# Optimization experiments

Hardware: AMD Instinct MI355X
Metric: run time of the kernel (lower is better)

Reference implementation:

```python
import jax, jax.numpy as jnp
import numpy as np


def _maxpool2(t):
    # 2x2x2 max pool, stride 2. t: [B, C, D, H, W]
    B, C, D, H, W = t.shape
    return t.reshape(B, C, D // 2, 2, H // 2, 2, W // 2, 2).max(axis=(3, 5, 7))


def setup_inputs() -> dict:
    key = jax.random.key(0)
    ks = jax.random.split(key, 5)
    ch = 64
    B, D, H, W = 2, 32, 32, 32
    x = jax.random.normal(ks[0], (B, ch, D, H, W), dtype=jnp.float32)
    # 1x1x1 conv weights (out_ch, in_ch), Kaiming-ish scale
    w_theta = jax.random.normal(ks[1], (ch // 8, ch), dtype=jnp.float32) / np.sqrt(ch)
    w_phi = jax.random.normal(ks[2], (ch // 8, ch), dtype=jnp.float32) / np.sqrt(ch)
    w_g = jax.random.normal(ks[3], (ch // 2, ch), dtype=jnp.float32) / np.sqrt(ch)
    w_o = jax.random.normal(ks[4], (ch, ch // 2), dtype=jnp.float32) / np.sqrt(ch // 2)
    gamma = jnp.ones((), dtype=jnp.float32)  # original inits at 0; 1 gives nontrivial output
    return {"x": x, "w_theta": w_theta, "w_phi": w_phi, "w_g": w_g, "w_o": w_o, "gamma": gamma}


def reference(x, w_theta, w_phi, w_g, w_o, gamma):
    B, C, D, H, W = x.shape
    N = D * H * W
    M = N // 8
    xf = x.reshape(B, C, N)  # [B, C, N]
    # 1x1x1 convs = channel matmuls
    theta = jnp.einsum('oc,bcn->bon', w_theta, xf)                     # [B, C//8, N]
    phi = _maxpool2(jnp.einsum('oc,bcn->bon', w_phi, xf).reshape(B, C // 8, D, H, W)).reshape(B, C // 8, M)
    g = _maxpool2(jnp.einsum('oc,bcn->bon', w_g, xf).reshape(B, C // 2, D, H, W)).reshape(B, C // 2, M)
    # unscaled attention: softmax over keys (M)
    beta = jax.nn.softmax(jnp.einsum('bcn,bcm->bnm', theta, phi), axis=-1)  # [B, N, M]
    o = jnp.einsum('bcm,bnm->bcn', g, beta)                                 # [B, C//2, N]
    out = gamma * jnp.einsum('oc,bcn->bon', w_o, o).reshape(B, C, D, H, W) + x
    return out
```

## Files before the change

kernel.cpp:

```cpp
#include <hip/hip_runtime.h>
#include <cstdint>
#include <cstddef>

typedef __attribute__((ext_vector_type(4))) short short4v;
typedef __attribute__((ext_vector_type(4))) float float4v;

#define C_IN  64
#define NB    2
#define NPTS  32768
#define MPTS  4096
#define LOG2E 1.44269504088896340736f
#define KT    64
#define NTILE (MPTS / KT)
#define QT64  (NPTS / 64)

__device__ __forceinline__ unsigned short f2bf_rne(float f) {
  unsigned int u = __builtin_bit_cast(unsigned int, f);
  u += 0x7fffu + ((u >> 16) & 1u);
  return (unsigned short)(u >> 16);
}

__device__ __forceinline__ short4v pack_bf16_trunc(float a0, float a1, float a2, float a3) {
  unsigned int u0 = __builtin_amdgcn_perm(__builtin_bit_cast(unsigned int, a1),
                                          __builtin_bit_cast(unsigned int, a0), 0x07060302u);
  unsigned int u1 = __builtin_amdgcn_perm(__builtin_bit_cast(unsigned int, a3),
                                          __builtin_bit_cast(unsigned int, a2), 0x07060302u);
  union { unsigned int u[2]; short4v s; } r;
  r.u[0] = u0; r.u[1] = u1;
  return r.s;
}

__device__ __forceinline__ short4v pack_bf16_rne(float a0, float a1, float a2, float a3) {
  short4v s;
  s[0] = (short)f2bf_rne(a0); s[1] = (short)f2bf_rne(a1);
  s[2] = (short)f2bf_rne(a2); s[3] = (short)f2bf_rne(a3);
  return s;
}

__device__ __forceinline__ uint2 pack_bf16x4_u2(float4v a) {
  uint2 r;
  r.x = (unsigned int)f2bf_rne(a[0]) | ((unsigned int)f2bf_rne(a[1]) << 16);
  r.y = (unsigned int)f2bf_rne(a[2]) | ((unsigned int)f2bf_rne(a[3]) << 16);
  return r;
}

__device__ __forceinline__ void unpack_bf16x4_add(uint2 u, float4v* a) {
  (*a)[0] += __builtin_bit_cast(float, u.x << 16);
  (*a)[1] += __builtin_bit_cast(float, u.x & 0xffff0000u);
  (*a)[2] += __builtin_bit_cast(float, u.y << 16);
  (*a)[3] += __builtin_bit_cast(float, u.y & 0xffff0000u);
}

__device__ __forceinline__ void gl_lds16(const unsigned short* g, unsigned short* l) {
  __builtin_amdgcn_global_load_lds(
      (const __attribute__((address_space(1))) void*)g,
      (__attribute__((address_space(3))) void*)l, 16, 0, 0);
}


__device__ void pool_body(int idx, const float* __restrict__ x,
                          const float* __restrict__ w_phi,
                          const float* __restrict__ w_g,
                          unsigned short* __restrict__ phi_f,
                          unsigned short* __restrict__ g_f) {
  int cg = idx >> 13;
  int bm = idx & 8191;
  int b = bm >> 12, m = bm & 4095;
  int md = m >> 8, mh = (m >> 4) & 15, mw = m & 15;
  const float* xb = x + (size_t)b * C_IN * NPTS
                  + ((md * 2) * 1024 + (mh * 2) * 32 + (mw * 2));
  const float* wbase = (cg < 2) ? (w_phi + cg * 4 * C_IN)
                                : (w_g + (cg - 2) * 4 * C_IN);

  float acc[4][8];
#pragma unroll
  for (int o = 0; o < 4; ++o)
#pragma unroll
    for (int p = 0; p < 8; ++p) acc[o][p] = 0.f;

#pragma unroll 4
  for (int cc = 0; cc < C_IN; ++cc) {
    const float* xp = xb + (size_t)cc * NPTS;
    float2 p01 = *(const float2*)(xp + 0);
    float2 p23 = *(const float2*)(xp + 32);
    float2 p45 = *(const float2*)(xp + 1024);
    float2 p67 = *(const float2*)(xp + 1056);
#pragma unroll
    for (int o = 0; o < 4; ++o) {
      float wv = wbase[o * C_IN + cc];
      acc[o][0] = fmaf(wv, p01.x, acc[o][0]);
      acc[o][1] = fmaf(wv, p01.y, acc[o][1]);
      acc[o][2] = fmaf(wv, p23.x, acc[o][2]);
      acc[o][3] = fmaf(wv, p23.y, acc[o][3]);
      acc[o][4] = fmaf(wv, p45.x, acc[o][4]);
      acc[o][5] = fmaf(wv, p45.y, acc[o][5]);
      acc[o][6] = fmaf(wv, p67.x, acc[o][6]);
      acc[o][7] = fmaf(wv, p67.y, acc[o][7]);
    }
  }
  float mx[4];
#pragma unroll
  for (int o = 0; o < 4; ++o) {
    mx[o] = fmaxf(fmaxf(fmaxf(acc[o][0], acc[o][1]), fmaxf(acc[o][2], acc[o][3])),
                  fmaxf(fmaxf(acc[o][4], acc[o][5]), fmaxf(acc[o][6], acc[o][7])));
  }
  int kt16 = m >> 4, kr = m & 15;
  if (cg < 2) {
    size_t fb = ((size_t)b * 256 + kt16) * 256;
    unsigned int u0 = (unsigned int)f2bf_rne(mx[0] * LOG2E)
                    | ((unsigned int)f2bf_rne(mx[1] * LOG2E) << 16);
    unsigned int u1 = (unsigned int)f2bf_rne(mx[2] * LOG2E)
                    | ((unsigned int)f2bf_rne(mx[3] * LOG2E) << 16);
    *(uint2*)&phi_f[fb + (cg * 16 + kr) * 4] = make_uint2(u0, u1);
    *(uint2*)&phi_f[fb + ((cg + 2) * 16 + kr) * 4] = make_uint2(0u, 0u);
  } else {
    int gc0 = (cg - 2) * 4;
#pragma unroll
    for (int o = 0; o < 4; ++o) {
      int c = gc0 + o;
      int half = c >> 4, c15 = c & 15;
      size_t base = (((size_t)b * 256 + kt16) * 2 + half) * 256;
      g_f[base + ((kr >> 2) * 16 + c15) * 4 + (kr & 3)] = f2bf_rne(mx[o]);
    }
  }
}

__device__ void theta_body(int idx, const float* __restrict__ x,
                           const float* __restrict__ w_theta,
                           unsigned short* __restrict__ theta_pad) {
  int b = idx >> 15, n = idx & 32767;
  const float* xb = x + (size_t)b * C_IN * NPTS + n;
  float t[8];
#pragma unroll
  for (int o = 0; o < 8; ++o) t[o] = 0.f;
#pragma unroll 4
  for (int cc = 0; cc < C_IN; ++cc) {
    float xv = xb[(size_t)cc * NPTS];
#pragma unroll
    for (int o = 0; o < 8; ++o) t[o] = fmaf(w_theta[o * C_IN + cc], xv, t[o]);
  }
  unsigned int w0 = (unsigned int)f2bf_rne(t[0]) | ((unsigned int)f2bf_rne(t[1]) << 16);
  unsigned int w1 = (unsigned int)f2bf_rne(t[2]) | ((unsigned int)f2bf_rne(t[3]) << 16);
  unsigned int w2 = (unsigned int)f2bf_rne(t[4]) | ((unsigned int)f2bf_rne(t[5]) << 16);
  unsigned int w3 = (unsigned int)f2bf_rne(t[6]) | ((unsigned int)f2bf_rne(t[7]) << 16);
  uint4* dst = (uint4*)(theta_pad + ((size_t)idx << 4));
  dst[0] = make_uint4(w0, w1, w2, w3);
  dst[1] = make_uint4(0u, 0u, 0u, 0u);
}

__global__ __launch_bounds__(256) void prep_fused(
    const float* __restrict__ x, const float* __restrict__ w_theta,
    const float* __restrict__ w_phi, const float* __restrict__ w_g,
    unsigned short* __restrict__ theta_pad,
    unsigned short* __restrict__ phi_f,
    unsigned short* __restrict__ g_f) {
  int gb = blockIdx.x;
  if (gb < 320) {
    pool_body(gb * 256 + threadIdx.x, x, w_phi, w_g, phi_f, g_f);
  } else {
    theta_body((gb - 320) * 256 + threadIdx.x, x, w_theta, theta_pad);
  }
}

template <int KS>
__global__ __launch_bounds__(256, 4) void attn_split64(
    const unsigned short* __restrict__ theta_pad,
    const unsigned short* __restrict__ phi_f,
    const unsigned short* __restrict__ g_f,
    uint2* __restrict__ opart,
    float* __restrict__ lbuf) {
  __shared__ unsigned short s_phi[2][KT * 16];
  __shared__ unsigned short s_g[2][(KT / 16) * 512];

  int tid = threadIdx.x;
  int wid = tid >> 6, lane = tid & 63;
  int l4 = lane >> 4, col = lane & 15;
  int b = blockIdx.y / KS;
  int ks = blockIdx.y % KS;
  int qb = blockIdx.x * 256 + wid * 64;
  int qt64 = blockIdx.x * 4 + wid;
  int t0 = ks * (NTILE / KS);
  int t1 = t0 + NTILE / KS;

  const unsigned short* tb = theta_pad + ((size_t)(b * NPTS + qb) << 4) + l4 * 4;
  short4v bt0 = *(const short4v*)(tb + ((0 * 16 + col) << 4));
  short4v bt1 = *(const short4v*)(tb + ((1 * 16 + col) << 4));
  short4v bt2 = *(const short4v*)(tb + ((2 * 16 + col) << 4));
  short4v bt3 = *(const short4v*)(tb + ((3 * 16 + col) << 4));

  const unsigned short* phib = phi_f + (size_t)b * 65536;
  const unsigned short* gb   = g_f + (size_t)b * 131072;

  float4v acc[2][4];
#pragma unroll
  for (int h = 0; h < 2; ++h)
#pragma unroll
    for (int j = 0; j < 4; ++j) acc[h][j] = (float4v){0.f, 0.f, 0.f, 0.f};
  float lsum0 = 0.f, lsum1 = 0.f, lsum2 = 0.f, lsum3 = 0.f;

  gl_lds16(gb + (size_t)t0 * 2048 + wid * 512 + lane * 8, &s_g[0][wid * 512]);
  if (wid < 2)
    gl_lds16(phib + (size_t)t0 * 1024 + wid * 512 + lane * 8, &s_phi[0][wid * 512]);
  __syncthreads();

#pragma unroll 1
  for (int t = t0; t < t1; ++t) {
    int cur = t & 1;
    if (t + 1 < t1) {
      gl_lds16(gb + (size_t)(t + 1) * 2048 + wid * 512 + lane * 8,
               &s_g[cur ^ 1][wid * 512]);
      if (wid < 2)
        gl_lds16(phib + (size_t)(t + 1) * 1024 + wid * 512 + lane * 8,
                 &s_phi[cur ^ 1][wid * 512]);
    }

#pragma unroll
    for (int st = 0; st < 4; ++st) {
      short4v pf = *(const short4v*)&s_phi[cur][st * 256 + lane * 4];
      short4v g0 = *(const short4v*)&s_g[cur][st * 512 + lane * 4];
      short4v g1 = *(const short4v*)&s_g[cur][st * 512 + 256 + lane * 4];

      float4v zero4 = {0.f, 0.f, 0.f, 0.f};
      float4v s0 = __builtin_amdgcn_mfma_f32_16x16x16bf16_1k(pf, bt0, zero4, 0, 0, 0);
      float4v s1 = __builtin_amdgcn_mfma_f32_16x16x16bf16_1k(pf, bt1, zero4, 0, 0, 0);
      float4v s2 = __builtin_amdgcn_mfma_f32_16x16x16bf16_1k(pf, bt2, zero4, 0, 0, 0);
      float4v s3 = __builtin_amdgcn_mfma_f32_16x16x16bf16_1k(pf, bt3, zero4, 0, 0, 0);

      float p00 = __builtin_amdgcn_exp2f(s0[0]);
      float p01 = __builtin_amdgcn_exp2f(s0[1]);
      float p02 = __builtin_amdgcn_exp2f(s0[2]);
      float p03 = __builtin_amdgcn_exp2f(s0[3]);
      float p10 = __builtin_amdgcn_exp2f(s1[0]);
      float p11 = __builtin_amdgcn_exp2f(s1[1]);
      float p12 = __builtin_amdgcn_exp2f(s1[2]);
      float p13 = __builtin_amdgcn_exp2f(s1[3]);
      float p20 = __builtin_amdgcn_exp2f(s2[0]);
      float p21 = __builtin_amdgcn_exp2f(s2[1]);
      float p22 = __builtin_amdgcn_exp2f(s2[2]);
      float p23 = __builtin_amdgcn_exp2f(s2[3]);
      float p30 = __builtin_amdgcn_exp2f(s3[0]);
      float p31 = __builtin_amdgcn_exp2f(s3[1]);
      float p32 = __builtin_amdgcn_exp2f(s3[2]);
      float p33 = __builtin_amdgcn_exp2f(s3[3]);
      lsum0 += (p00 + p01) + (p02 + p03);
      lsum1 += (p10 + p11) + (p12 + p13);
      lsum2 += (p20 + p21) + (p22 + p23);
      lsum3 += (p30 + p31) + (p32 + p33);
      short4v pb0 = pack_bf16_trunc(p00, p01, p02, p03);
      short4v pb1 = pack_bf16_trunc(p10, p11, p12, p13);
      short4v pb2 = pack_bf16_trunc(p20, p21, p22, p23);
      short4v pb3 = pack_bf16_trunc(p30, p31, p32, p33);

      acc[0][0] = __builtin_amdgcn_mfma_f32_16x16x16bf16_1k(g0, pb0, acc[0][0], 0, 0, 0);
      acc[0][1] = __builtin_amdgcn_mfma_f32_16x16x16bf16_1k(g0, pb1, acc[0][1], 0, 0, 0);
      acc[0][2] = __builtin_amdgcn_mfma_f32_16x16x16bf16_1k(g0, pb2, acc[0][2], 0, 0, 0);
      acc[0][3] = __builtin_amdgcn_mfma_f32_16x16x16bf16_1k(g0, pb3, acc[0][3], 0, 0, 0);
      acc[1][0] = __builtin_amdgcn_mfma_f32_16x16x16bf16_1k(g1, pb0, acc[1][0], 0, 0, 0);
      acc[1][1] = __builtin_amdgcn_mfma_f32_16x16x16bf16_1k(g1, pb1, acc[1][1], 0, 0, 0);
      acc[1][2] = __builtin_amdgcn_mfma_f32_16x16x16bf16_1k(g1, pb2, acc[1][2], 0, 0, 0);
      acc[1][3] = __builtin_amdgcn_mfma_f32_16x16x16bf16_1k(g1, pb3, acc[1][3], 0, 0, 0);
    }
    __syncthreads();
  }

  lsum0 += __shfl_xor(lsum0, 16, 64);
  lsum0 += __shfl_xor(lsum0, 32, 64);
  lsum1 += __shfl_xor(lsum1, 16, 64);
  lsum1 += __shfl_xor(lsum1, 32, 64);
  lsum2 += __shfl_xor(lsum2, 16, 64);
  lsum2 += __shfl_xor(lsum2, 32, 64);
  lsum3 += __shfl_xor(lsum3, 16, 64);
  lsum3 += __shfl_xor(lsum3, 32, 64);

  size_t rowb = (size_t)(b * KS + ks) * QT64 + qt64;
  float myl = (l4 == 0) ? lsum0 : (l4 == 1) ? lsum1 : (l4 == 2) ? lsum2 : lsum3;
  lbuf[rowb * 64 + lane] = myl;

  size_t obase = rowb * 8 * 64 + lane;
#pragma unroll
  for (int h = 0; h < 2; ++h)
#pragma unroll
    for (int j = 0; j < 4; ++j)
      opart[obase + (size_t)(h * 4 + j) * 64] = pack_bf16x4_u2(acc[h][j]);
}

template <int KS>
__global__ __launch_bounds__(256) void attn_combine(
    const float* __restrict__ x, const float* __restrict__ w_o,
    const float* __restrict__ gamma_p,
    const uint2* __restrict__ opart,
    const float* __restrict__ lbuf,
    float* __restrict__ out) {
  int tid = threadIdx.x;
  int wid = tid >> 6, lane = tid & 63;
  int l4 = lane >> 4, col = lane & 15;
  int b = blockIdx.y;
  int qt32 = blockIdx.x * 4 + wid;
  int qb = qt32 * 32;
  int qt64 = qt32 >> 1, hf = qt32 & 1;

  float gamma = gamma_p[0];

  short4v wo[4][2];
#pragma unroll
  for (int cot = 0; cot < 4; ++cot)
#pragma unroll
    for (int ksw = 0; ksw < 2; ++ksw) {
      const float* wp = w_o + (cot * 16 + col) * 32 + ksw * 16 + l4 * 4;
      wo[cot][ksw] = pack_bf16_rne(wp[0] * gamma, wp[1] * gamma,
                                   wp[2] * gamma, wp[3] * gamma);
    }

  float4v a0 = {0.f, 0.f, 0.f, 0.f}, a1 = a0, a2 = a0, a3 = a0;
  float ls0 = 0.f, ls1 = 0.f;
#pragma unroll
  for (int ks = 0; ks < KS; ++ks) {
    size_t rowb = (size_t)(b * KS + ks) * QT64 + qt64;
    size_t ob = (rowb * 8 + hf * 2) * 64 + lane;
    unpack_bf16x4_add(opart[ob + 0 * 64], &a0);
    unpack_bf16x4_add(opart[ob + 1 * 64], &a1);
    unpack_bf16x4_add(opart[ob + 4 * 64], &a2);
    unpack_bf16x4_add(opart[ob + 5 * 64], &a3);
    const float* lb = lbuf + rowb * 64 + hf * 32;
    ls0 += lb[col];
    ls1 += lb[col + 16];
  }
  float li0 = 1.0f / ls0;
  float li1 = 1.0f / ls1;

  short4v onb00 = pack_bf16_rne(a0[0] * li0, a0[1] * li0, a0[2] * li0, a0[3] * li0);
  short4v onb01 = pack_bf16_rne(a1[0] * li1, a1[1] * li1, a1[2] * li1, a1[3] * li1);
  short4v onb10 = pack_bf16_rne(a2[0] * li0, a2[1] * li0, a2[2] * li0, a2[3] * li0);
  short4v onb11 = pack_bf16_rne(a3[0] * li1, a3[1] * li1, a3[2] * li1, a3[3] * li1);

  float4v zero4 = {0.f, 0.f, 0.f, 0.f};
#pragma unroll
  for (int cot = 0; cot < 4; ++cot) {
#pragma unroll
    for (int nt = 0; nt < 2; ++nt) {
      short4v bfrag0 = nt ? onb01 : onb00;
      short4v bfrag1 = nt ? onb11 : onb10;
      float4v d = __builtin_amdgcn_mfma_f32_16x16x16bf16_1k(wo[cot][0], bfrag0, zero4, 0, 0, 0);
      d = __builtin_amdgcn_mfma_f32_16x16x16bf16_1k(wo[cot][1], bfrag1, d, 0, 0, 0);
      int n = qb + nt * 16 + col;
      size_t base = (size_t)(b * C_IN + cot * 16 + l4 * 4) * NPTS + n;
      const float* xp = x + base;
      float* op = out + base;
#pragma unroll
      for (int e = 0; e < 4; ++e) {
        op[(size_t)e * NPTS] = d[e] + xp[(size_t)e * NPTS];
      }
    }
  }
}

__global__ __launch_bounds__(256) void attn_mfma(
    const float* __restrict__ x, const float* __restrict__ w_o,
    const float* __restrict__ gamma_p,
    const unsigned short* __restrict__ theta_pad,
    const unsigned short* __restrict__ phi_f,
    const unsigned short* __restrict__ g_f,
    float* __restrict__ out) {
  __shared__ unsigned short s_phi[2][KT * 16];
  __shared__ unsigned short s_g[2][(KT / 16) * 512];

  int tid = threadIdx.x;
  int wid = tid >> 6, lane = tid & 63;
  int l4 = lane >> 4, col = lane & 15;
  int b = blockIdx.y;
  int qb = blockIdx.x * 128 + wid * 32;

  float gamma = gamma_p[0];

  const unsigned short* tb = theta_pad + ((size_t)(b * NPTS + qb) << 4) + l4 * 4;
  short4v bt0 = *(const short4v*)(tb + (col << 4));
  short4v bt1 = *(const short4v*)(tb + ((16 + col) << 4));

  short4v wo[4][2];
#pragma unroll
  for (int cot = 0; cot < 4; ++cot)
#pragma unroll
    for (int ksw = 0; ksw < 2; ++ksw) {
      const float* wp = w_o + (cot * 16 + col) * 32 + ksw * 16 + l4 * 4;
      wo[cot][ksw] = pack_bf16_rne(wp[0] * gamma, wp[1] * gamma,
                                   wp[2] * gamma, wp[3] * gamma);
    }

  const unsigned short* phib = phi_f + (size_t)b * 256 * 256;
  const unsigned short* gb   = g_f + (size_t)b * 256 * 512;

  float4v acc00 = {0.f, 0.f, 0.f, 0.f}, acc01 = acc00, acc10 = acc00, acc11 = acc00;
  float lsum0 = 0.f, lsum1 = 0.f;

  gl_lds16(gb + 0 * 2048 + wid * 512 + lane * 8, &s_g[0][wid * 512]);
  if (wid < 2)
    gl_lds16(phib + 0 * 1024 + wid * 512 + lane * 8, &s_phi[0][wid * 512]);
  __syncthreads();

#pragma unroll 1
  for (int t = 0; t < NTILE; ++t) {
    int cur = t & 1;
    if (t + 1 < NTILE) {
      gl_lds16(gb + (size_t)(t + 1) * 2048 + wid * 512 + lane * 8,
               &s_g[cur ^ 1][wid * 512]);
      if (wid < 2)
        gl_lds16(phib + (size_t)(t + 1) * 1024 + wid * 512 + lane * 8,
                 &s_phi[cur ^ 1][wid * 512]);
    }
#pragma unroll
    for (int st = 0; st < 4; ++st) {
      short4v pf = *(const short4v*)&s_phi[cur][st * 256 + lane * 4];
      short4v g0 = *(const short4v*)&s_g[cur][st * 512 + lane * 4];
      short4v g1 = *(const short4v*)&s_g[cur][st * 512 + 256 + lane * 4];

      float4v zero4 = {0.f, 0.f, 0.f, 0.f};
      float4v s0 = __builtin_amdgcn_mfma_f32_16x16x16bf16_1k(pf, bt0, zero4, 0, 0, 0);
      float4v s1 = __builtin_amdgcn_mfma_f32_16x16x16bf16_1k(pf, bt1, zero4, 0, 0, 0);

      float p00 = __builtin_amdgcn_exp2f(s0[0]);
      float p01 = __builtin_amdgcn_exp2f(s0[1]);
      float p02 = __builtin_amdgcn_exp2f(s0[2]);
      float p03 = __builtin_amdgcn_exp2f(s0[3]);
      float p10 = __builtin_amdgcn_exp2f(s1[0]);
      float p11 = __builtin_amdgcn_exp2f(s1[1]);
      float p12 = __builtin_amdgcn_exp2f(s1[2]);
      float p13 = __builtin_amdgcn_exp2f(s1[3]);
      lsum0 += (p00 + p01) + (p02 + p03);
      lsum1 += (p10 + p11) + (p12 + p13);
      short4v pb0 = pack_bf16_trunc(p00, p01, p02, p03);
      short4v pb1 = pack_bf16_trunc(p10, p11, p12, p13);

      acc00 = __builtin_amdgcn_mfma_f32_16x16x16bf16_1k(g0, pb0, acc00, 0, 0, 0);
      acc01 = __builtin_amdgcn_mfma_f32_16x16x16bf16_1k(g0, pb1, acc01, 0, 0, 0);
      acc10 = __builtin_amdgcn_mfma_f32_16x16x16bf16_1k(g1, pb0, acc10, 0, 0, 0);
      acc11 = __builtin_amdgcn_mfma_f32_16x16x16bf16_1k(g1, pb1, acc11, 0, 0, 0);
    }
    __syncthreads();
  }

  lsum0 += __shfl_xor(lsum0, 16, 64);
  lsum0 += __shfl_xor(lsum0, 32, 64);
  lsum1 += __shfl_xor(lsum1, 16, 64);
  lsum1 += __shfl_xor(lsum1, 32, 64);
  float li0 = 1.0f / lsum0;
  float li1 = 1.0f / lsum1;

  short4v onb00 = pack_bf16_rne(acc00[0] * li0, acc00[1] * li0, acc00[2] * li0, acc00[3] * li0);
  short4v onb01 = pack_bf16_rne(acc01[0] * li1, acc01[1] * li1, acc01[2] * li1, acc01[3] * li1);
  short4v onb10 = pack_bf16_rne(acc10[0] * li0, acc10[1] * li0, acc10[2] * li0, acc10[3] * li0);
  short4v onb11 = pack_bf16_rne(acc11[0] * li1, acc11[1] * li1, acc11[2] * li1, acc11[3] * li1);

  float4v zero4 = {0.f, 0.f, 0.f, 0.f};
#pragma unroll
  for (int cot = 0; cot < 4; ++cot) {
#pragma unroll
    for (int nt = 0; nt < 2; ++nt) {
      short4v bfrag0 = nt ? onb01 : onb00;
      short4v bfrag1 = nt ? onb11 : onb10;
      float4v d = __builtin_amdgcn_mfma_f32_16x16x16bf16_1k(wo[cot][0], bfrag0, zero4, 0, 0, 0);
      d = __builtin_amdgcn_mfma_f32_16x16x16bf16_1k(wo[cot][1], bfrag1, d, 0, 0, 0);
      int n = qb + nt * 16 + col;
      size_t base = (size_t)(b * C_IN + cot * 16 + l4 * 4) * NPTS + n;
      const float* xp = x + base;
      float* op = out + base;
#pragma unroll
      for (int e = 0; e < 4; ++e) {
        op[(size_t)e * NPTS] = d[e] + xp[(size_t)e * NPTS];
      }
    }
  }
}

extern "C" void kernel_launch(void* const* d_in, const int* in_sizes, int n_in,
                              void* d_out, int out_size, void* d_ws, size_t ws_size,
                              hipStream_t stream) {
  const float* x       = (const float*)d_in[0];
  const float* w_theta = (const float*)d_in[1];
  const float* w_phi   = (const float*)d_in[2];
  const float* w_g     = (const float*)d_in[3];
  const float* w_o     = (const float*)d_in[4];
  const float* gamma   = (const float*)d_in[5];
  float* out = (float*)d_out;

  char* ws = (char*)d_ws;
  unsigned short* phi_f     = (unsigned short*)ws;  ws += (size_t)NB * 256 * 256 * 2;
  unsigned short* g_f       = (unsigned short*)ws;  ws += (size_t)NB * 256 * 512 * 2;
  unsigned short* theta_pad = (unsigned short*)ws;  ws += (size_t)NB * NPTS * 16 * 2;
  size_t base_need = (size_t)(ws - (char*)d_ws);
  uint2* opart = (uint2*)ws;
  size_t opart4 = (size_t)NB * 4 * QT64 * 8 * 64 * sizeof(uint2);
  size_t opart2 = (size_t)NB * 2 * QT64 * 8 * 64 * sizeof(uint2);
  size_t lbuf4  = (size_t)NB * 4 * QT64 * 64 * sizeof(float);
  size_t lbuf2  = (size_t)NB * 2 * QT64 * 64 * sizeof(float);
  size_t need4 = base_need + opart4 + lbuf4;
  size_t need2 = base_need + opart2 + lbuf2;

  prep_fused<<<dim3(576), dim3(256), 0, stream>>>(
      x, w_theta, w_phi, w_g, theta_pad, phi_f, g_f);

  if (ws_size >= need4) {
    float* lbuf = (float*)((char*)opart + opart4);
    attn_split64<4><<<dim3(NPTS / 256, NB * 4), dim3(256), 0, stream>>>(
        theta_pad, phi_f, g_f, opart, lbuf);
    attn_combine<4><<<dim3(NPTS / 128, NB), dim3(256), 0, stream>>>(
        x, w_o, gamma, opart, lbuf, out);
  } else if (ws_size >= need2) {
    float* lbuf = (float*)((char*)opart + opart2);
    attn_split64<2><<<dim3(NPTS / 256, NB * 2), dim3(256), 0, stream>>>(
        theta_pad, phi_f, g_f, opart, lbuf);
    attn_combine<2><<<dim3(NPTS / 128, NB), dim3(256), 0, stream>>>(
        x, w_o, gamma, opart, lbuf, out);
  } else if (ws_size >= base_need) {
    attn_mfma<<<dim3(NPTS / 128, NB), dim3(256), 0, stream>>>(
        x, w_o, gamma, theta_pad, phi_f, g_f, out);
  }
}
```

Baseline: 80.83 us.

## Triple-buffer phi/g tiles with two-deep prefetch and vmcnt-based waits

Replaces the double-buffered LDS staging in the attention kernel with a three-buffer ring, prefetching two tiles ahead and issuing the next load after compute. Each iteration now waits with an explicit s_waitcnt vmcnt followed by a single barrier, instead of a __syncthreads at the end of every tile. All four waves now issue phi loads (duplicated writes for waves 2-3) so that vmcnt counts stay uniform. The aim is to hide global-to-LDS latency and cut barrier stalls, at the cost of more LDS per block, which may reduce occupancy.

After: 78.93 us, median of 2. 2.4% less time.

```diff
diff --git a/kernel.cpp b/kernel.cpp
--- a/kernel.cpp
+++ b/kernel.cpp
@@ -169,8 +169,8 @@
     const unsigned short* __restrict__ g_f,
     uint2* __restrict__ opart,
     float* __restrict__ lbuf) {
-  __shared__ unsigned short s_phi[2][KT * 16];
-  __shared__ unsigned short s_g[2][(KT / 16) * 512];
+  __shared__ unsigned short s_phi[3][KT * 16];
+  __shared__ unsigned short s_g[3][(KT / 16) * 512];
 
   int tid = threadIdx.x;
   int wid = tid >> 6, lane = tid & 63;
@@ -180,7 +180,7 @@
   int qb = blockIdx.x * 256 + wid * 64;
   int qt64 = blockIdx.x * 4 + wid;
   int t0 = ks * (NTILE / KS);
-  int t1 = t0 + NTILE / KS;
+  const int T = NTILE / KS;
 
   const unsigned short* tb = theta_pad + ((size_t)(b * NPTS + qb) << 4) + l4 * 4;
   short4v bt0 = *(const short4v*)(tb + ((0 * 16 + col) << 4));
@@ -198,21 +198,27 @@
     for (int j = 0; j < 4; ++j) acc[h][j] = (float4v){0.f, 0.f, 0.f, 0.f};
   float lsum0 = 0.f, lsum1 = 0.f, lsum2 = 0.f, lsum3 = 0.f;
 
-  gl_lds16(gb + (size_t)t0 * 2048 + wid * 512 + lane * 8, &s_g[0][wid * 512]);
-  if (wid < 2)
-    gl_lds16(phib + (size_t)t0 * 1024 + wid * 512 + lane * 8, &s_phi[0][wid * 512]);
-  __syncthreads();
-
+#define STAGE(tt, bb)                                                          \
+  do {                                                                         \
+    gl_lds16(gb + (size_t)(tt) * 2048 + wid * 512 + lane * 8,                  \
+             &s_g[bb][wid * 512]);                                             \
+    gl_lds16(phib + (size_t)(tt) * 1024 + (wid & 1) * 512 + lane * 8,          \
+             &s_phi[bb][(wid & 1) * 512]);                                     \
+  } while (0)
+
+  STAGE(t0, 0);
+  STAGE(t0 + 1, 1);
+
+  int cur = 0;
 #pragma unroll 1
-  for (int t = t0; t < t1; ++t) {
-    int cur = t & 1;
-    if (t + 1 < t1) {
-      gl_lds16(gb + (size_t)(t + 1) * 2048 + wid * 512 + lane * 8,
-               &s_g[cur ^ 1][wid * 512]);
-      if (wid < 2)
-        gl_lds16(phib + (size_t)(t + 1) * 1024 + wid * 512 + lane * 8,
-                 &s_phi[cur ^ 1][wid * 512]);
-    }
+  for (int i = 0; i < T; ++i) {
+    if (i + 1 < T) {
+      asm volatile("s_waitcnt vmcnt(2)" ::: "memory");
+    } else {
+      asm volatile("s_waitcnt vmcnt(0)" ::: "memory");
+    }
+    __builtin_amdgcn_s_barrier();
+    __builtin_amdgcn_sched_barrier(0);
 
 #pragma unroll
     for (int st = 0; st < 4; ++st) {
@@ -260,8 +266,14 @@
       acc[1][2] = __builtin_amdgcn_mfma_f32_16x16x16bf16_1k(g1, pb2, acc[1][2], 0, 0, 0);
       acc[1][3] = __builtin_amdgcn_mfma_f32_16x16x16bf16_1k(g1, pb3, acc[1][3], 0, 0, 0);
     }
-    __syncthreads();
-  }
+
+    if (i + 2 < T) {
+      int bb = (cur + 2 >= 3) ? cur - 1 : cur + 2;
+      STAGE(t0 + i + 2, bb);
+    }
+    cur = (cur == 2) ? 0 : cur + 1;
+  }
+#undef STAGE
 
   lsum0 += __shfl_xor(lsum0, 16, 64);
   lsum0 += __shfl_xor(lsum0, 32, 64);
```
